# Kernel optimization log

Measured on AMD Instinct MI355X. Metric: run time of the kernel, lower is better.

## Reference

```python
import jax, jax.numpy as jnp
import numpy as np

B, T, C = 4, 2048, 1024
NH = 16
HD = C // NH

def setup_inputs() -> dict:
    key = jax.random.key(0)
    k1, k2, k3 = jax.random.split(key, 3)
    x = jax.random.normal(k1, (B, T, C), dtype=jnp.float32)
    w_attn = jax.random.normal(k2, (C, 3 * C), dtype=jnp.float32) * (1.0 / np.sqrt(C))
    w_proj = jax.random.normal(k3, (C, C), dtype=jnp.float32) * (1.0 / np.sqrt(C))
    return {"x": x, "w_attn": w_attn, "w_proj": w_proj}

def reference(x, w_attn, w_proj):
    b, t, c = x.shape
    qkv = x @ w_attn  # [B,T,3C]
    q, k, v = jnp.split(qkv, 3, axis=-1)
    # [B,T,C] -> [B,NH,T,HD]
    def heads(a):
        return a.reshape(b, t, NH, HD).transpose(0, 2, 1, 3)
    q, k, v = heads(q), heads(k), heads(v)
    scale = 1.0 / np.sqrt(HD)
    att = jnp.einsum('bhqd,bhkd->bhqk', q, k) * scale  # materialized TxT scores
    causal = jnp.tril(jnp.ones((t, t), dtype=bool))
    att = jnp.where(causal, att, -jnp.inf)
    att = jax.nn.softmax(att, axis=-1)
    y = jnp.einsum('bhqk,bhkd->bhqd', att, v)
    y = y.transpose(0, 2, 1, 3).reshape(b, t, c)
    return y @ w_proj
```

## Files before the change

kernel.cpp:

```cpp
#include <hip/hip_runtime.h>

typedef unsigned short u16;
typedef short bf16x8 __attribute__((ext_vector_type(8)));
typedef float f32x4 __attribute__((ext_vector_type(4)));
typedef float f32x16 __attribute__((ext_vector_type(16)));

#define B_  4
#define T_  2048
#define C_  1024
#define NH_ 16
#define HD_ 64

__device__ __forceinline__ void gload16(const u16* g, u16* lds) {
  __builtin_amdgcn_global_load_lds(
      (const __attribute__((address_space(1))) void*)g,
      (__attribute__((address_space(3))) void*)lds, 16, 0, 0);
}

__device__ __forceinline__ u16 f2bf(float f) {
  union { float f; unsigned u; } x; x.f = f;
  unsigned r = x.u + 0x7fffu + ((x.u >> 16) & 1u);
  return (u16)(r >> 16);
}

#define PSWAP(a, b) asm("v_permlane32_swap_b32 %0, %1" : "+v"(a), "+v"(b))

__global__ __launch_bounds__(256) void convert_x(const float* __restrict__ in,
                                                 u16* __restrict__ out) {
  int i = (blockIdx.x * 256 + threadIdx.x) * 8;
  float4 a = *(const float4*)(in + i);
  float4 b = *(const float4*)(in + i + 4);
  u16 t[8] = {f2bf(a.x), f2bf(a.y), f2bf(a.z), f2bf(a.w),
              f2bf(b.x), f2bf(b.y), f2bf(b.z), f2bf(b.w)};
  *(uint4*)(out + i) = *(const uint4*)t;
}

__global__ __launch_bounds__(256) void transpose_w(const float* __restrict__ in,
                                                   u16* __restrict__ out,
                                                   int R, int Cc) {
  int r0 = blockIdx.x * 64, c0 = blockIdx.y * 64;
  __shared__ __attribute__((aligned(16))) u16 tile[64][72];
  int tid = threadIdx.x;
#pragma unroll
  for (int it = 0; it < 4; ++it) {
    int chunk = it * 256 + tid;
    int row = chunk >> 4, c4 = chunk & 15;
    float4 v = *(const float4*)(in + (size_t)(r0 + row) * Cc + c0 + c4 * 4);
    tile[row][c4 * 4 + 0] = f2bf(v.x);
    tile[row][c4 * 4 + 1] = f2bf(v.y);
    tile[row][c4 * 4 + 2] = f2bf(v.z);
    tile[row][c4 * 4 + 3] = f2bf(v.w);
  }
  __syncthreads();
#pragma unroll
  for (int it = 0; it < 2; ++it) {
    int chunk = it * 256 + tid;
    int row = chunk >> 3, c8 = chunk & 7;
    uint4 v; u16* tv = (u16*)&v;
#pragma unroll
    for (int k = 0; k < 8; ++k) tv[k] = tile[c8 * 8 + k][row];
    *(uint4*)(out + (size_t)(c0 + row) * R + r0 + c8 * 8) = v;
  }
}

__device__ __forceinline__ void gemm_bt_tile(const u16* __restrict__ A,
                                             const u16* __restrict__ Bt,
                                             int Kdim, int m0, int n0,
                                             u16* sA, u16* sB, f32x4 acc[4][4]) {
  int tid = threadIdx.x;
  int w = tid >> 6, l = tid & 63, li = l & 15, quad = l >> 4;
  int wm = (w >> 1) * 64, wn = (w & 1) * 64;
  f32x4 zero = {0.f, 0.f, 0.f, 0.f};
#pragma unroll
  for (int i = 0; i < 4; ++i)
#pragma unroll
    for (int j = 0; j < 4; ++j) acc[i][j] = zero;

  for (int k0 = 0; k0 < Kdim; k0 += 32) {
#pragma unroll
    for (int r = 0; r < 2; ++r) {
      int chunk = r * 256 + tid;
      int row = chunk >> 2, c8 = chunk & 3;
      gload16(A  + (size_t)(m0 + row) * Kdim + k0 + c8 * 8, sA + chunk * 8);
      gload16(Bt + (size_t)(n0 + row) * Kdim + k0 + c8 * 8, sB + chunk * 8);
    }
    __syncthreads();
    bf16x8 af[4], bfr[4];
#pragma unroll
    for (int i = 0; i < 4; ++i)
      af[i] = *(const bf16x8*)(sA + (wm + i * 16 + li) * 32 + quad * 8);
#pragma unroll
    for (int j = 0; j < 4; ++j)
      bfr[j] = *(const bf16x8*)(sB + (wn + j * 16 + li) * 32 + quad * 8);
#pragma unroll
    for (int i = 0; i < 4; ++i)
#pragma unroll
      for (int j = 0; j < 4; ++j)
        acc[i][j] = __builtin_amdgcn_mfma_f32_16x16x32_bf16(af[i], bfr[j], acc[i][j], 0, 0, 0);
    __syncthreads();
  }
}

__global__ __launch_bounds__(256) void gemm_qkv(const u16* __restrict__ X,
                                                const u16* __restrict__ WT,
                                                u16* __restrict__ Qb,
                                                u16* __restrict__ Kb,
                                                u16* __restrict__ Vt) {
  __shared__ __attribute__((aligned(16))) u16 sA[128 * 32];
  __shared__ __attribute__((aligned(16))) u16 sB[128 * 32];
  f32x4 acc[4][4];
  int m0 = blockIdx.x * 128, n0 = blockIdx.y * 128;
  gemm_bt_tile(X, WT, C_, m0, n0, sA, sB, acc);

  int tid = threadIdx.x;
  int w = tid >> 6, l = tid & 63, li = l & 15, quad = l >> 4;
  int wm = (w >> 1) * 64, wn = (w & 1) * 64;
#pragma unroll
  for (int i = 0; i < 4; ++i)
#pragma unroll
    for (int j = 0; j < 4; ++j) {
      int n = n0 + wn + j * 16 + li;
      int which = n >> 10, cc = n & (C_ - 1);
      int h = cc >> 6, d = cc & (HD_ - 1);
      int mb = m0 + wm + i * 16 + quad * 4;
      int b = mb >> 11, t0 = mb & (T_ - 1);
      if (which == 2) {
        u16 tv[4] = {f2bf(acc[i][j][0]), f2bf(acc[i][j][1]),
                     f2bf(acc[i][j][2]), f2bf(acc[i][j][3])};
        *(uint2*)(Vt + ((size_t)(b * NH_ + h) * HD_ + d) * T_ + t0) = *(const uint2*)tv;
      } else {
        u16* dst = (which == 0) ? Qb : Kb;
#pragma unroll
        for (int r = 0; r < 4; ++r)
          dst[((size_t)(b * NH_ + h) * T_ + t0 + r) * HD_ + d] = f2bf(acc[i][j][r]);
      }
    }
}

__global__ __launch_bounds__(256) void gemm_proj(const u16* __restrict__ Y,
                                                 const u16* __restrict__ WT,
                                                 float* __restrict__ Out) {
  __shared__ __attribute__((aligned(16))) u16 sA[128 * 32];
  __shared__ __attribute__((aligned(16))) u16 sB[128 * 32];
  f32x4 acc[4][4];
  int m0 = blockIdx.x * 128, n0 = blockIdx.y * 128;
  gemm_bt_tile(Y, WT, C_, m0, n0, sA, sB, acc);

  int tid = threadIdx.x;
  int w = tid >> 6, l = tid & 63, li = l & 15, quad = l >> 4;
  int wm = (w >> 1) * 64, wn = (w & 1) * 64;
#pragma unroll
  for (int i = 0; i < 4; ++i)
#pragma unroll
    for (int j = 0; j < 4; ++j)
#pragma unroll
      for (int r = 0; r < 4; ++r) {
        int m = m0 + wm + i * 16 + quad * 4 + r;
        int n = n0 + wn + j * 16 + li;
        Out[(size_t)m * C_ + n] = acc[i][j][r];
      }
}

__global__ __launch_bounds__(256, 2) void attn_k(const u16* __restrict__ Q,
                                                 const u16* __restrict__ K,
                                                 const u16* __restrict__ Vt,
                                                 u16* __restrict__ Y) {
  int bh = blockIdx.x;
  int qt = 7 - (int)blockIdx.y;
  int tid = threadIdx.x;
  int w = tid >> 6, l = tid & 63;
  int l31 = l & 31, hi = l >> 5;
  int qrow_base = qt * 256 + w * 64;

  __shared__ __attribute__((aligned(16))) u16 sK[2][64 * 64];
  __shared__ __attribute__((aligned(16))) u16 sV[2][64 * 64];

  const u16* kbase = K + (size_t)bh * T_ * HD_;
  const u16* vbase = Vt + (size_t)bh * HD_ * T_;

  bf16x8 qf[2][4];
#pragma unroll
  for (int qs = 0; qs < 2; ++qs) {
    const u16* qp = Q + ((size_t)bh * T_ + qrow_base + qs * 32 + l31) * HD_ + hi * 8;
#pragma unroll
    for (int c = 0; c < 4; ++c) qf[qs][c] = *(const bf16x8*)(qp + c * 16);
  }

  f32x16 o[2][2];
#pragma unroll
  for (int qs = 0; qs < 2; ++qs)
#pragma unroll
    for (int dt = 0; dt < 2; ++dt)
#pragma unroll
      for (int r = 0; r < 16; ++r) o[qs][dt][r] = 0.f;
  float mrow[2] = {-1e30f, -1e30f};
  float lsum[2] = {0.f, 0.f};
  const float csc = 0.125f * 1.44269504088896f;

  int nkv = 4 * qt + 4;

#define STAGE(buf, kv0_)                                                      \
  {                                                                           \
    _Pragma("unroll")                                                         \
    for (int rr = 0; rr < 2; ++rr) {                                          \
      int chunk = rr * 256 + tid;                                             \
      int row = chunk >> 3;                                                   \
      int cs = ((chunk & 7) ^ (row & 7)) * 8;                                 \
      gload16(kbase + (size_t)((kv0_) + row) * HD_ + cs, sK[buf] + chunk * 8);\
      gload16(vbase + (size_t)row * T_ + (kv0_) + cs, sV[buf] + chunk * 8);   \
    }                                                                         \
  }

  STAGE(0, 0);
  __syncthreads();

  int cur = 0;
  for (int kvt = 0; kvt < nkv; ++kvt) {
    int kv0 = kvt * 64;
    if (kvt + 1 < nkv) STAGE(cur ^ 1, kv0 + 64);

    unsigned u[2][16];
    bool aq[2], a1[2];
#pragma unroll
    for (int qs = 0; qs < 2; ++qs) {
      aq[qs] = (kv0 <= qrow_base + qs * 32 + 31);
      a1[qs] = (kv0 + 32 <= qrow_base + qs * 32 + 31);
    }

    if (aq[1]) {
      bf16x8 kf[2][4];
#pragma unroll
      for (int c = 0; c < 4; ++c) {
        int row = l31;
        int c16 = (2 * c + hi) ^ (row & 7);
        kf[0][c] = *(const bf16x8*)(sK[cur] + row * 64 + c16 * 8);
      }
      if (a1[1]) {
#pragma unroll
        for (int c = 0; c < 4; ++c) {
          int row = 32 + l31;
          int c16 = (2 * c + hi) ^ (row & 7);
          kf[1][c] = *(const bf16x8*)(sK[cur] + row * 64 + c16 * 8);
        }
      }

#pragma unroll
      for (int qs = 0; qs < 2; ++qs) {
        if (!aq[qs]) continue;
        int qb = qrow_base + qs * 32;
        int qg = qb + l31;

        f32x16 st0, st1;
#pragma unroll
        for (int r = 0; r < 16; ++r) { st0[r] = 0.f; st1[r] = 0.f; }
        __builtin_amdgcn_s_setprio(1);
#pragma unroll
        for (int c = 0; c < 4; ++c)
          st0 = __builtin_amdgcn_mfma_f32_32x32x16_bf16(kf[0][c], qf[qs][c], st0, 0, 0, 0);
        if (a1[qs]) {
#pragma unroll
          for (int c = 0; c < 4; ++c)
            st1 = __builtin_amdgcn_mfma_f32_32x32x16_bf16(kf[1][c], qf[qs][c], st1, 0, 0, 0);
        }
        __builtin_amdgcn_s_setprio(0);

        if (kv0 + 63 > qb) {
#pragma unroll
          for (int r = 0; r < 16; ++r) {
            int kvg = kv0 + (r & 3) + 8 * (r >> 2) + 4 * hi;
            if (kvg > qg) st0[r] = -1e30f;
            if (a1[qs] && kvg + 32 > qg) st1[r] = -1e30f;
          }
        }

        float ml = st0[0];
#pragma unroll
        for (int r = 1; r < 16; ++r) ml = fmaxf(ml, st0[r]);
        if (a1[qs]) {
#pragma unroll
          for (int r = 0; r < 16; ++r) ml = fmaxf(ml, st1[r]);
        }
        float mt = fmaxf(ml, __shfl_xor(ml, 32));
        float g = (mt - mrow[qs]) * csc;
        if (!__all(g <= 8.0f)) {
          float mnew = fmaxf(mrow[qs], mt);
          float alpha = exp2f((mrow[qs] - mnew) * csc);
          mrow[qs] = mnew;
          lsum[qs] *= alpha;
#pragma unroll
          for (int r = 0; r < 16; ++r) {
            int qlr = (r & 3) + 8 * (r >> 2) + 4 * hi;
            float ar = __shfl(alpha, qlr);
            o[qs][0][r] *= ar;
            o[qs][1][r] *= ar;
          }
        }

        float mc = mrow[qs] * csc;
        float ls = 0.f;
#pragma unroll
        for (int r = 0; r < 16; ++r) {
          float p = exp2f(__builtin_fmaf(st0[r], csc, -mc));
          ls += p; st0[r] = p;
        }
        if (a1[qs]) {
#pragma unroll
          for (int r = 0; r < 16; ++r) {
            float p = exp2f(__builtin_fmaf(st1[r], csc, -mc));
            ls += p; st1[r] = p;
          }
        }
        lsum[qs] += ls;

#pragma unroll
        for (int k = 0; k < 8; ++k)
          asm("v_cvt_pk_bf16_f32 %0, %1, %2"
              : "=v"(u[qs][k]) : "v"(st0[2 * k]), "v"(st0[2 * k + 1]));
        if (a1[qs]) {
#pragma unroll
          for (int k = 0; k < 8; ++k)
            asm("v_cvt_pk_bf16_f32 %0, %1, %2"
                : "=v"(u[qs][8 + k]) : "v"(st1[2 * k]), "v"(st1[2 * k + 1]));
        }
#pragma unroll
        for (int h2 = 0; h2 < 2; ++h2) {
          PSWAP(u[qs][4 * h2 + 0], u[qs][4 * h2 + 2]);
          PSWAP(u[qs][4 * h2 + 1], u[qs][4 * h2 + 3]);
        }
        if (a1[qs]) {
#pragma unroll
          for (int h2 = 0; h2 < 2; ++h2) {
            PSWAP(u[qs][8 + 4 * h2 + 0], u[qs][8 + 4 * h2 + 2]);
            PSWAP(u[qs][8 + 4 * h2 + 1], u[qs][8 + 4 * h2 + 3]);
          }
        }
      }

      __builtin_amdgcn_s_setprio(1);
#pragma unroll
      for (int dt = 0; dt < 2; ++dt) {
        bf16x8 vf[4];
#pragma unroll
        for (int c = 0; c < 4; ++c) {
          int row = 32 * dt + l31;
          int c16 = (2 * c + hi) ^ (row & 7);
          vf[c] = *(const bf16x8*)(sV[cur] + row * 64 + c16 * 8);
        }
#pragma unroll
        for (int qs = 0; qs < 2; ++qs) {
          if (!aq[qs]) continue;
#pragma unroll
          for (int c = 0; c < 4; ++c) {
            if (c >= 2 && !a1[qs]) continue;
            union { unsigned uu[4]; bf16x8 v; } pa;
            pa.uu[0] = u[qs][8 * (c >> 1) + 4 * (c & 1) + 0];
            pa.uu[1] = u[qs][8 * (c >> 1) + 4 * (c & 1) + 1];
            pa.uu[2] = u[qs][8 * (c >> 1) + 4 * (c & 1) + 2];
            pa.uu[3] = u[qs][8 * (c >> 1) + 4 * (c & 1) + 3];
            o[qs][dt] = __builtin_amdgcn_mfma_f32_32x32x16_bf16(pa.v, vf[c], o[qs][dt], 0, 0, 0);
          }
        }
      }
      __builtin_amdgcn_s_setprio(0);
    }

    __syncthreads();
    cur ^= 1;
  }

  int b = bh >> 4, h = bh & (NH_ - 1);
#pragma unroll
  for (int qs = 0; qs < 2; ++qs) {
    float lt = lsum[qs] + __shfl_xor(lsum[qs], 32);
    float rv = 1.0f / fmaxf(lt, 1e-20f);
#pragma unroll
    for (int r = 0; r < 16; ++r) {
      int qlr = (r & 3) + 8 * (r >> 2) + 4 * hi;
      float rr = __shfl(rv, qlr);
      int qg = qrow_base + qs * 32 + qlr;
      size_t base = ((size_t)b * T_ + qg) * C_ + h * HD_;
      Y[base + l31]      = f2bf(o[qs][0][r] * rr);
      Y[base + 32 + l31] = f2bf(o[qs][1][r] * rr);
    }
  }
#undef STAGE
}

extern "C" void kernel_launch(void* const* d_in, const int* in_sizes, int n_in,
                              void* d_out, int out_size, void* d_ws, size_t ws_size,
                              hipStream_t stream) {
  (void)in_sizes; (void)n_in; (void)out_size; (void)ws_size;
  const float* x      = (const float*)d_in[0];
  const float* w_attn = (const float*)d_in[1];
  const float* w_proj = (const float*)d_in[2];
  float* out = (float*)d_out;

  const size_t NTOK = (size_t)B_ * T_ * C_;
  u16* watT   = (u16*)d_ws;
  u16* wprojT = watT   + (size_t)3 * C_ * C_;
  u16* xbf    = wprojT + (size_t)C_ * C_;
  u16* qb     = xbf  + NTOK;
  u16* kb     = qb   + NTOK;
  u16* vtb    = kb   + NTOK;
  u16* yb     = xbf;

  transpose_w<<<dim3(16, 48), 256, 0, stream>>>(w_attn, watT, C_, 3 * C_);
  transpose_w<<<dim3(16, 16), 256, 0, stream>>>(w_proj, wprojT, C_, C_);
  convert_x<<<dim3(4096), 256, 0, stream>>>(x, xbf);
  gemm_qkv<<<dim3(64, 24), 256, 0, stream>>>(xbf, watT, qb, kb, vtb);
  attn_k<<<dim3(64, 8), 256, 0, stream>>>(qb, kb, vtb, yb);
  gemm_proj<<<dim3(64, 8), 256, 0, stream>>>(yb, wprojT, out);
}
```

Measured before the change: 282.8 us.

## Shrink attention query tile to 128 rows and raise occupancy to 4 blocks

Each attention block now covers 128 query rows, 32 per wave, where it used to cover 256. The grid doubles to 64x16 and launch bounds allow 4 blocks per CU. Halving the per-wave state (one Q fragment set, one output accumulator pair) is meant to free registers and add parallelism, which should improve latency hiding and causal load balance. Staging now uses precomputed offsets with pointer bumps, and the P fragments are kept in a union instead of being repacked. In exchange, each K/V tile loaded into LDS is reused by fewer query rows, so total K/V traffic roughly doubles.

Measured after the change: 290.5 us. 1.03x slower.

```diff
diff --git a/kernel.cpp b/kernel.cpp
--- a/kernel.cpp
+++ b/kernel.cpp
@@ -161,16 +161,17 @@
       }
 }
 
-__global__ __launch_bounds__(256, 2) void attn_k(const u16* __restrict__ Q,
+__global__ __launch_bounds__(256, 4) void attn_k(const u16* __restrict__ Q,
                                                  const u16* __restrict__ K,
                                                  const u16* __restrict__ Vt,
                                                  u16* __restrict__ Y) {
   int bh = blockIdx.x;
-  int qt = 7 - (int)blockIdx.y;
+  int qt = 15 - (int)blockIdx.y;
   int tid = threadIdx.x;
   int w = tid >> 6, l = tid & 63;
   int l31 = l & 31, hi = l >> 5;
-  int qrow_base = qt * 256 + w * 64;
+  int qb = qt * 128 + w * 32;
+  int qg = qb + l31;
 
   __shared__ __attribute__((aligned(16))) u16 sK[2][64 * 64];
   __shared__ __attribute__((aligned(16))) u16 sV[2][64 * 64];
@@ -178,161 +179,156 @@
   const u16* kbase = K + (size_t)bh * T_ * HD_;
   const u16* vbase = Vt + (size_t)bh * HD_ * T_;
 
-  bf16x8 qf[2][4];
-#pragma unroll
-  for (int qs = 0; qs < 2; ++qs) {
-    const u16* qp = Q + ((size_t)bh * T_ + qrow_base + qs * 32 + l31) * HD_ + hi * 8;
-#pragma unroll
-    for (int c = 0; c < 4; ++c) qf[qs][c] = *(const bf16x8*)(qp + c * 16);
-  }
-
-  f32x16 o[2][2];
-#pragma unroll
-  for (int qs = 0; qs < 2; ++qs)
-#pragma unroll
-    for (int dt = 0; dt < 2; ++dt)
-#pragma unroll
-      for (int r = 0; r < 16; ++r) o[qs][dt][r] = 0.f;
-  float mrow[2] = {-1e30f, -1e30f};
-  float lsum[2] = {0.f, 0.f};
+  bf16x8 qf[4];
+  {
+    const u16* qp = Q + ((size_t)bh * T_ + qg) * HD_ + hi * 8;
+#pragma unroll
+    for (int c = 0; c < 4; ++c) qf[c] = *(const bf16x8*)(qp + c * 16);
+  }
+
+  f32x16 o[2];
+#pragma unroll
+  for (int dt = 0; dt < 2; ++dt)
+#pragma unroll
+    for (int r = 0; r < 16; ++r) o[dt][r] = 0.f;
+  float mrow = -1e30f, lsum = 0.f;
   const float csc = 0.125f * 1.44269504088896f;
 
-  int nkv = 4 * qt + 4;
-
-#define STAGE(buf, kv0_)                                                      \
-  {                                                                           \
-    _Pragma("unroll")                                                         \
-    for (int rr = 0; rr < 2; ++rr) {                                          \
-      int chunk = rr * 256 + tid;                                             \
-      int row = chunk >> 3;                                                   \
-      int cs = ((chunk & 7) ^ (row & 7)) * 8;                                 \
-      gload16(kbase + (size_t)((kv0_) + row) * HD_ + cs, sK[buf] + chunk * 8);\
-      gload16(vbase + (size_t)row * T_ + (kv0_) + cs, sV[buf] + chunk * 8);   \
-    }                                                                         \
-  }
-
-  STAGE(0, 0);
+  int nkv = 2 * qt + 2;
+
+  int koff[2], voff[2], ldst[2];
+  {
+    int r0 = tid >> 3, c0_ = tid & 7;
+#pragma unroll
+    for (int rr = 0; rr < 2; ++rr) {
+      int row = rr * 32 + r0;
+      int cs = (c0_ ^ (row & 7)) * 8;
+      koff[rr] = row * HD_ + cs;
+      voff[rr] = row * T_ + cs;
+      ldst[rr] = (rr * 256 + tid) * 8;
+    }
+  }
+  const u16* kst = kbase;
+  const u16* vst = vbase;
+#define STAGE(buf)                                        \
+  {                                                       \
+    gload16(kst + koff[0], sK[buf] + ldst[0]);            \
+    gload16(vst + voff[0], sV[buf] + ldst[0]);            \
+    gload16(kst + koff[1], sK[buf] + ldst[1]);            \
+    gload16(vst + voff[1], sV[buf] + ldst[1]);            \
+    kst += 64 * HD_; vst += 64;                           \
+  }
+
+  STAGE(0);
   __syncthreads();
 
   int cur = 0;
   for (int kvt = 0; kvt < nkv; ++kvt) {
     int kv0 = kvt * 64;
-    if (kvt + 1 < nkv) STAGE(cur ^ 1, kv0 + 64);
-
-    unsigned u[2][16];
-    bool aq[2], a1[2];
-#pragma unroll
-    for (int qs = 0; qs < 2; ++qs) {
-      aq[qs] = (kv0 <= qrow_base + qs * 32 + 31);
-      a1[qs] = (kv0 + 32 <= qrow_base + qs * 32 + 31);
-    }
-
-    if (aq[1]) {
-      bf16x8 kf[2][4];
+    if (kvt + 1 < nkv) STAGE(cur ^ 1);
+
+    bool aq = (kv0 <= qb + 31);
+    bool a1 = (kv0 + 32 <= qb + 31);
+    if (aq) {
+      bf16x8 kf0[4], kf1[4];
 #pragma unroll
       for (int c = 0; c < 4; ++c) {
         int row = l31;
         int c16 = (2 * c + hi) ^ (row & 7);
-        kf[0][c] = *(const bf16x8*)(sK[cur] + row * 64 + c16 * 8);
-      }
-      if (a1[1]) {
+        kf0[c] = *(const bf16x8*)(sK[cur] + row * 64 + c16 * 8);
+      }
+      if (a1) {
 #pragma unroll
         for (int c = 0; c < 4; ++c) {
           int row = 32 + l31;
           int c16 = (2 * c + hi) ^ (row & 7);
-          kf[1][c] = *(const bf16x8*)(sK[cur] + row * 64 + c16 * 8);
-        }
-      }
-
-#pragma unroll
-      for (int qs = 0; qs < 2; ++qs) {
-        if (!aq[qs]) continue;
-        int qb = qrow_base + qs * 32;
-        int qg = qb + l31;
-
-        f32x16 st0, st1;
-#pragma unroll
-        for (int r = 0; r < 16; ++r) { st0[r] = 0.f; st1[r] = 0.f; }
-        __builtin_amdgcn_s_setprio(1);
+          kf1[c] = *(const bf16x8*)(sK[cur] + row * 64 + c16 * 8);
+        }
+      }
+
+      f32x16 st0, st1;
+#pragma unroll
+      for (int r = 0; r < 16; ++r) { st0[r] = 0.f; st1[r] = 0.f; }
+      __builtin_amdgcn_s_setprio(1);
+#pragma unroll
+      for (int c = 0; c < 4; ++c)
+        st0 = __builtin_amdgcn_mfma_f32_32x32x16_bf16(kf0[c], qf[c], st0, 0, 0, 0);
+      if (a1) {
 #pragma unroll
         for (int c = 0; c < 4; ++c)
-          st0 = __builtin_amdgcn_mfma_f32_32x32x16_bf16(kf[0][c], qf[qs][c], st0, 0, 0, 0);
-        if (a1[qs]) {
-#pragma unroll
-          for (int c = 0; c < 4; ++c)
-            st1 = __builtin_amdgcn_mfma_f32_32x32x16_bf16(kf[1][c], qf[qs][c], st1, 0, 0, 0);
-        }
-        __builtin_amdgcn_s_setprio(0);
-
-        if (kv0 + 63 > qb) {
-#pragma unroll
-          for (int r = 0; r < 16; ++r) {
-            int kvg = kv0 + (r & 3) + 8 * (r >> 2) + 4 * hi;
-            if (kvg > qg) st0[r] = -1e30f;
-            if (a1[qs] && kvg + 32 > qg) st1[r] = -1e30f;
-          }
-        }
-
-        float ml = st0[0];
-#pragma unroll
-        for (int r = 1; r < 16; ++r) ml = fmaxf(ml, st0[r]);
-        if (a1[qs]) {
-#pragma unroll
-          for (int r = 0; r < 16; ++r) ml = fmaxf(ml, st1[r]);
-        }
-        float mt = fmaxf(ml, __shfl_xor(ml, 32));
-        float g = (mt - mrow[qs]) * csc;
-        if (!__all(g <= 8.0f)) {
-          float mnew = fmaxf(mrow[qs], mt);
-          float alpha = exp2f((mrow[qs] - mnew) * csc);
-          mrow[qs] = mnew;
-          lsum[qs] *= alpha;
-#pragma unroll
-          for (int r = 0; r < 16; ++r) {
-            int qlr = (r & 3) + 8 * (r >> 2) + 4 * hi;
-            float ar = __shfl(alpha, qlr);
-            o[qs][0][r] *= ar;
-            o[qs][1][r] *= ar;
-          }
-        }
-
-        float mc = mrow[qs] * csc;
-        float ls = 0.f;
+          st1 = __builtin_amdgcn_mfma_f32_32x32x16_bf16(kf1[c], qf[c], st1, 0, 0, 0);
+      }
+      __builtin_amdgcn_s_setprio(0);
+
+      if (kv0 + 63 > qb) {
 #pragma unroll
         for (int r = 0; r < 16; ++r) {
-          float p = exp2f(__builtin_fmaf(st0[r], csc, -mc));
-          ls += p; st0[r] = p;
-        }
-        if (a1[qs]) {
-#pragma unroll
-          for (int r = 0; r < 16; ++r) {
-            float p = exp2f(__builtin_fmaf(st1[r], csc, -mc));
-            ls += p; st1[r] = p;
-          }
-        }
-        lsum[qs] += ls;
-
+          int kvg = kv0 + (r & 3) + 8 * (r >> 2) + 4 * hi;
+          if (kvg > qg) st0[r] = -1e30f;
+          if (a1 && kvg + 32 > qg) st1[r] = -1e30f;
+        }
+      }
+
+      float ml = st0[0];
+#pragma unroll
+      for (int r = 1; r < 16; ++r) ml = fmaxf(ml, st0[r]);
+      if (a1) {
+#pragma unroll
+        for (int r = 0; r < 16; ++r) ml = fmaxf(ml, st1[r]);
+      }
+      float mt = fmaxf(ml, __shfl_xor(ml, 32));
+      float g = (mt - mrow) * csc;
+      if (!__all(g <= 8.0f)) {
+        float mnew = fmaxf(mrow, mt);
+        float alpha = exp2f((mrow - mnew) * csc);
+        mrow = mnew;
+        lsum *= alpha;
+#pragma unroll
+        for (int r = 0; r < 16; ++r) {
+          int qlr = (r & 3) + 8 * (r >> 2) + 4 * hi;
+          float ar = __shfl(alpha, qlr);
+          o[0][r] *= ar;
+          o[1][r] *= ar;
+        }
+      }
+
+      float mc = mrow * csc;
+      float ls = 0.f;
+#pragma unroll
+      for (int r = 0; r < 16; ++r) {
+        float p = exp2f(__builtin_fmaf(st0[r], csc, -mc));
+        ls += p; st0[r] = p;
+      }
+      if (a1) {
+#pragma unroll
+        for (int r = 0; r < 16; ++r) {
+          float p = exp2f(__builtin_fmaf(st1[r], csc, -mc));
+          ls += p; st1[r] = p;
+        }
+      }
+      lsum += ls;
+
+      union { unsigned uu[16]; bf16x8 v[4]; } pu;
+#pragma unroll
+      for (int k = 0; k < 8; ++k)
+        asm("v_cvt_pk_bf16_f32 %0, %1, %2"
+            : "=v"(pu.uu[k]) : "v"(st0[2 * k]), "v"(st0[2 * k + 1]));
+      if (a1) {
 #pragma unroll
         for (int k = 0; k < 8; ++k)
           asm("v_cvt_pk_bf16_f32 %0, %1, %2"
-              : "=v"(u[qs][k]) : "v"(st0[2 * k]), "v"(st0[2 * k + 1]));
-        if (a1[qs]) {
-#pragma unroll
-          for (int k = 0; k < 8; ++k)
-            asm("v_cvt_pk_bf16_f32 %0, %1, %2"
-                : "=v"(u[qs][8 + k]) : "v"(st1[2 * k]), "v"(st1[2 * k + 1]));
-        }
+              : "=v"(pu.uu[8 + k]) : "v"(st1[2 * k]), "v"(st1[2 * k + 1]));
+      }
+#pragma unroll
+      for (int h2 = 0; h2 < 2; ++h2) {
+        PSWAP(pu.uu[4 * h2 + 0], pu.uu[4 * h2 + 2]);
+        PSWAP(pu.uu[4 * h2 + 1], pu.uu[4 * h2 + 3]);
+      }
+      if (a1) {
 #pragma unroll
         for (int h2 = 0; h2 < 2; ++h2) {
-          PSWAP(u[qs][4 * h2 + 0], u[qs][4 * h2 + 2]);
-          PSWAP(u[qs][4 * h2 + 1], u[qs][4 * h2 + 3]);
-        }
-        if (a1[qs]) {
-#pragma unroll
-          for (int h2 = 0; h2 < 2; ++h2) {
-            PSWAP(u[qs][8 + 4 * h2 + 0], u[qs][8 + 4 * h2 + 2]);
-            PSWAP(u[qs][8 + 4 * h2 + 1], u[qs][8 + 4 * h2 + 3]);
-          }
+          PSWAP(pu.uu[8 + 4 * h2 + 0], pu.uu[8 + 4 * h2 + 2]);
+          PSWAP(pu.uu[8 + 4 * h2 + 1], pu.uu[8 + 4 * h2 + 3]);
         }
       }
 
@@ -347,18 +343,9 @@
           vf[c] = *(const bf16x8*)(sV[cur] + row * 64 + c16 * 8);
         }
 #pragma unroll
-        for (int qs = 0; qs < 2; ++qs) {
-          if (!aq[qs]) continue;
-#pragma unroll
-          for (int c = 0; c < 4; ++c) {
-            if (c >= 2 && !a1[qs]) continue;
-            union { unsigned uu[4]; bf16x8 v; } pa;
-            pa.uu[0] = u[qs][8 * (c >> 1) + 4 * (c & 1) + 0];
-            pa.uu[1] = u[qs][8 * (c >> 1) + 4 * (c & 1) + 1];
-            pa.uu[2] = u[qs][8 * (c >> 1) + 4 * (c & 1) + 2];
-            pa.uu[3] = u[qs][8 * (c >> 1) + 4 * (c & 1) + 3];
-            o[qs][dt] = __builtin_amdgcn_mfma_f32_32x32x16_bf16(pa.v, vf[c], o[qs][dt], 0, 0, 0);
-          }
+        for (int c = 0; c < 4; ++c) {
+          if (c >= 2 && !a1) continue;
+          o[dt] = __builtin_amdgcn_mfma_f32_32x32x16_bf16(pu.v[c], vf[c], o[dt], 0, 0, 0);
         }
       }
       __builtin_amdgcn_s_setprio(0);
@@ -369,19 +356,16 @@
   }
 
   int b = bh >> 4, h = bh & (NH_ - 1);
-#pragma unroll
-  for (int qs = 0; qs < 2; ++qs) {
-    float lt = lsum[qs] + __shfl_xor(lsum[qs], 32);
-    float rv = 1.0f / fmaxf(lt, 1e-20f);
-#pragma unroll
-    for (int r = 0; r < 16; ++r) {
-      int qlr = (r & 3) + 8 * (r >> 2) + 4 * hi;
-      float rr = __shfl(rv, qlr);
-      int qg = qrow_base + qs * 32 + qlr;
-      size_t base = ((size_t)b * T_ + qg) * C_ + h * HD_;
-      Y[base + l31]      = f2bf(o[qs][0][r] * rr);
-      Y[base + 32 + l31] = f2bf(o[qs][1][r] * rr);
-    }
+  float lt = lsum + __shfl_xor(lsum, 32);
+  float rv = 1.0f / fmaxf(lt, 1e-20f);
+#pragma unroll
+  for (int r = 0; r < 16; ++r) {
+    int qlr = (r & 3) + 8 * (r >> 2) + 4 * hi;
+    float rr = __shfl(rv, qlr);
+    int qq = qb + qlr;
+    size_t base = ((size_t)b * T_ + qq) * C_ + h * HD_;
+    Y[base + l31]      = f2bf(o[0][r] * rr);
+    Y[base + 32 + l31] = f2bf(o[1][r] * rr);
   }
 #undef STAGE
 }
@@ -408,6 +392,6 @@
   transpose_w<<<dim3(16, 16), 256, 0, stream>>>(w_proj, wprojT, C_, C_);
   convert_x<<<dim3(4096), 256, 0, stream>>>(x, xbf);
   gemm_qkv<<<dim3(64, 24), 256, 0, stream>>>(xbf, watT, qb, kb, vtb);
-  attn_k<<<dim3(64, 8), 256, 0, stream>>>(qb, kb, vtb, yb);
+  attn_k<<<dim3(64, 16), 256, 0, stream>>>(qb, kb, vtb, yb);
   gemm_proj<<<dim3(64, 8), 256, 0, stream>>>(yb, wprojT, out);
 }
```
